# Optimization experiments

Hardware: AMD Instinct MI355X
Metric: run time of the kernel (lower is better)

## Reference

```python
import jax, jax.numpy as jnp
import numpy as np
from jax import lax

# Resolved Optuna hyperparameters
NPOINTS = (512, 256, 128)
RADII = (0.2, 0.4, 0.8)
KS = (32, 32, 32)
BN_EPS = 1e-5


def _fps_single(pts, npoint):
    """Farthest point sampling on one cloud. pts: (N,3) -> (npoint,) int32."""
    N = pts.shape[0]
    def step(carry, _):
        dists, last = carry
        d = jnp.sum((pts - pts[last]) ** 2, axis=-1)
        dists = jnp.minimum(dists, d)
        nxt = jnp.argmax(dists).astype(jnp.int32)
        return (dists, nxt), last
    init = (jnp.full((N,), 1e10, pts.dtype), jnp.int32(0))
    (_, _), idx = lax.scan(step, init, None, length=npoint)
    return idx


def _set_abstraction(xyz, feat, W, b, radius, k, npoint):
    """xyz: (B,N,3), feat: (B,N,C_in) -> new_xyz (B,S,3), new_feat (B,S,C_out)."""
    B, N, _ = xyz.shape
    fps_idx = jax.vmap(lambda p: _fps_single(p, npoint))(xyz)          # (B,S)
    new_xyz = jax.vmap(lambda x, i: x[i])(xyz, fps_idx)                # (B,S,3)
    # ball query: squared distances centers -> all points
    d2 = jnp.sum((new_xyz[:, :, None, :] - xyz[:, None, :, :]) ** 2, axis=-1)  # (B,S,N)
    valid = d2 <= radius * radius
    ar = jnp.arange(N, dtype=jnp.int32)
    gi = jnp.where(valid, ar[None, None, :], N)                        # invalid -> N
    gi = jnp.sort(gi, axis=-1)[:, :, :k]                               # first k in index order
    first = gi[:, :, :1]
    gi = jnp.where(gi == N, first, gi)                                 # pad with first valid (center itself)
    g_xyz = jax.vmap(lambda x, i: x[i])(xyz, gi)                       # (B,S,k,3)
    rel = g_xyz - new_xyz[:, :, None, :]
    g_feat = jax.vmap(lambda x, i: x[i])(feat, gi)                     # (B,S,k,C_in)
    h = jnp.concatenate([rel, g_feat], axis=-1)                        # (B,S,k,3+C_in)
    h = jax.nn.relu(jnp.einsum('bskc,co->bsko', h, W) + b)
    return new_xyz, jnp.max(h, axis=2)                                 # max-pool over group


def _bn(x, g, b):
    # nn.BatchNorm1d training-mode forward (batch statistics, biased var)
    m = x.mean(axis=0)
    v = x.var(axis=0)
    return (x - m) * lax.rsqrt(v + BN_EPS) * g + b


def setup_inputs() -> dict:
    key = jax.random.key(0)
    ks = jax.random.split(key, 8)
    def w(k, i, o):
        return (jax.random.normal(k, (i, o), jnp.float32) / np.sqrt(i)).astype(jnp.float32)
    return dict(
        points=jax.random.uniform(ks[0], (16, 4096, 3), jnp.float32),
        W1=w(ks[1], 3 + 3, 64),   b1=jnp.zeros((64,), jnp.float32),
        W2=w(ks[2], 64 + 3, 128), b2=jnp.zeros((128,), jnp.float32),
        W3=w(ks[3], 128 + 3, 256), b3=jnp.zeros((256,), jnp.float32),
        fc1_w=w(ks[4], 256, 256), fc1_b=jnp.zeros((256,), jnp.float32),
        fc2_w=w(ks[5], 256, 128), fc2_b=jnp.zeros((128,), jnp.float32),
        fc3_w=w(ks[6], 128, 12),  fc3_b=jnp.zeros((12,), jnp.float32),
        bn1_g=jnp.ones((256,), jnp.float32), bn1_b=jnp.zeros((256,), jnp.float32),
        bn2_g=jnp.ones((128,), jnp.float32), bn2_b=jnp.zeros((128,), jnp.float32),
    )


def reference(points, W1, b1, W2, b2, W3, b3, fc1_w, fc1_b, fc2_w, fc2_b,
              fc3_w, fc3_b, bn1_g, bn1_b, bn2_g, bn2_b):
    B = points.shape[0]
    xyz, feat = points, points
    for (W, bb, r, k, s) in ((W1, b1, RADII[0], KS[0], NPOINTS[0]),
                             (W2, b2, RADII[1], KS[1], NPOINTS[1]),
                             (W3, b3, RADII[2], KS[2], NPOINTS[2])):
        xyz, feat = _set_abstraction(xyz, feat, W, bb, r, k, s)
    f = jnp.max(feat, axis=1)                                          # (B, ch3)
    x = jax.nn.relu(_bn(f @ fc1_w + fc1_b, bn1_g, bn1_b))              # dropout: eval-mode identity
    x = jax.nn.relu(_bn(x @ fc2_w + fc2_b, bn2_g, bn2_b))
    x = x @ fc3_w + fc3_b
    return x.reshape(B, 4, 3)
```

## Files before the change

### kernel.cpp

```cpp
#include <hip/hip_runtime.h>
#include <hip/hip_bf16.h>


#define B_SZ 16

template<int CTRL>
__device__ __forceinline__ float dpp_mv(float v) {
    const int i = __float_as_int(v);
    const int r = __builtin_amdgcn_update_dpp(i, i, CTRL, 0xf, 0xf, false);
    return __int_as_float(r);
}

__device__ __forceinline__ float wave_max_f32(float x) {
    float v = x;
    v = fmaxf(v, dpp_mv<0x111>(v));
    v = fmaxf(v, dpp_mv<0x112>(v));
    v = fmaxf(v, dpp_mv<0x114>(v));
    v = fmaxf(v, dpp_mv<0x118>(v));
    v = fmaxf(v, dpp_mv<0x142>(v));
    v = fmaxf(v, dpp_mv<0x143>(v));
    return __uint_as_float(__builtin_amdgcn_readlane(__float_as_uint(v), 63));
}

__device__ __forceinline__ float read_lane_f32(float v, int l) {
    return __uint_as_float(__builtin_amdgcn_readlane(__float_as_uint(v), l));
}

template<int N, int NPOINT, int BLOCK, int S0, int S1, bool FIRST>
__global__ __launch_bounds__(BLOCK) void fps_kernel(
    const float* __restrict__ xyz,
    float* __restrict__ newxyz,
    float* __restrict__ dstate)
{
    constexpr int P  = N / BLOCK;
    constexpr int NW = BLOCK / 64;
    constexpr int O0 = FIRST ? 0 : S0;
    __shared__ float4 part[2][NW];
    __shared__ float  outb[(S1 - O0) * 3];

    const int b = blockIdx.x, tid = threadIdx.x;
    const int lane = tid & 63, w = tid >> 6;
    const float* xb = xyz + (size_t)b * N * 3;

    float px[P], py[P], pz[P], dd[P];
    const int base = tid * P;
#pragma unroll
    for (int i = 0; i < P; i++) {
        px[i] = xb[(base + i) * 3 + 0];
        py[i] = xb[(base + i) * 3 + 1];
        pz[i] = xb[(base + i) * 3 + 2];
    }
    float lx, ly, lz;
    if (FIRST) {
#pragma unroll
        for (int i = 0; i < P; i++) dd[i] = 1e10f;
        lx = xb[0]; ly = xb[1]; lz = xb[2];
        if (tid == 0) { outb[0] = lx; outb[1] = ly; outb[2] = lz; }
    } else {
#pragma unroll
        for (int i = 0; i < P; i++) dd[i] = dstate[((size_t)b * P + i) * BLOCK + tid];
        const float* c = newxyz + ((size_t)b * NPOINT + (S0 - 1)) * 3;
        lx = c[0]; ly = c[1]; lz = c[2];
    }

    for (int s = S0; s < S1; s++) {
        float bv = -1.0f, bx = 0.0f, by = 0.0f, bz = 0.0f;
#pragma unroll
        for (int i = 0; i < P; i++) {
            const float dx = px[i] - lx, dy = py[i] - ly, dz = pz[i] - lz;
            const float d2 = __fadd_rn(__fadd_rn(__fmul_rn(dx, dx), __fmul_rn(dy, dy)),
                                       __fmul_rn(dz, dz));
            const float nd = fminf(dd[i], d2);
            dd[i] = nd;
            const bool gt = nd > bv;
            bv = gt ? nd : bv;
            bx = gt ? px[i] : bx;
            by = gt ? py[i] : by;
            bz = gt ? pz[i] : bz;
        }
        const float wmax = wave_max_f32(bv);
        const unsigned long long mset = __ballot(bv == wmax);
        const int li = __ffsll(mset) - 1;
        const int buf = s & 1;
        if (lane == li) part[buf][w] = make_float4(bv, bx, by, bz);
        __syncthreads();
        float cv = -1.0f;
#pragma unroll
        for (int q = 0; q < NW; q++) {
            const float4 pq = part[buf][q];
            const bool gt = pq.x > cv;
            cv = gt ? pq.x : cv;
            lx = gt ? pq.y : lx;
            ly = gt ? pq.z : ly;
            lz = gt ? pq.w : lz;
        }
        if (tid == 0) {
            const int t = (s - O0) * 3;
            outb[t + 0] = lx; outb[t + 1] = ly; outb[t + 2] = lz;
        }
    }
    __syncthreads();
    if (S1 < NPOINT) {
#pragma unroll
        for (int i = 0; i < P; i++)
            dstate[((size_t)b * P + i) * BLOCK + tid] = dd[i];
    }
    float* o = newxyz + ((size_t)b * NPOINT + O0) * 3;
    for (int t = tid; t < (S1 - O0) * 3; t += BLOCK) o[t] = outb[t];
}

template<int N, int NPOINT>
__device__ __forceinline__ void fps_wave_body(
    const float* __restrict__ xyz,
    float* __restrict__ newxyz,
    const int b, const int lane)
{
    constexpr int P = N / 64;
    const float* xb = xyz + (size_t)b * N * 3;

    float px[P], py[P], pz[P], dd[P];
    const int base = lane * P;
#pragma unroll
    for (int i = 0; i < P; i++) {
        px[i] = xb[(base + i) * 3 + 0];
        py[i] = xb[(base + i) * 3 + 1];
        pz[i] = xb[(base + i) * 3 + 2];
        dd[i] = 1e10f;
    }
#pragma unroll
    for (int i = 0; i < P; i++) {
        asm volatile("" : "+v"(px[i]), "+v"(py[i]), "+v"(pz[i]));
    }
    float lx = xb[0], ly = xb[1], lz = xb[2];
    if (lane == 0) {
        float* o = newxyz + (size_t)b * NPOINT * 3;
        o[0] = lx; o[1] = ly; o[2] = lz;
    }

    for (int s = 1; s < NPOINT; s++) {
        float bv = -1.0f, bx = 0.0f, by = 0.0f, bz = 0.0f;
#pragma unroll
        for (int i = 0; i < P; i++) {
            const float dx = px[i] - lx, dy = py[i] - ly, dz = pz[i] - lz;
            const float d2 = __fadd_rn(__fadd_rn(__fmul_rn(dx, dx), __fmul_rn(dy, dy)),
                                       __fmul_rn(dz, dz));
            const float nd = fminf(dd[i], d2);
            dd[i] = nd;
            const bool gt = nd > bv;
            bv = gt ? nd : bv;
            bx = gt ? px[i] : bx;
            by = gt ? py[i] : by;
            bz = gt ? pz[i] : bz;
        }
        const float wmax = wave_max_f32(bv);
        const unsigned long long mset = __ballot(bv == wmax);
        const int li = __ffsll(mset) - 1;
        lx = read_lane_f32(bx, li);
        ly = read_lane_f32(by, li);
        lz = read_lane_f32(bz, li);
        if (lane == 0) {
            float* o = newxyz + ((size_t)b * NPOINT + s) * 3;
            o[0] = lx; o[1] = ly; o[2] = lz;
        }
    }
}

template<int N, int S, int CF, int COUT, int R, bool AMAX>
__device__ __forceinline__ void sa_body(
    const float* __restrict__ xyz,
    const float* __restrict__ feat,
    const float* __restrict__ cent,
    const float* __restrict__ W,
    const float* __restrict__ bias,
    float* __restrict__ outf,
    const float r2, const int s, const int b, const int lane)
{
    constexpr int K    = 32;
    constexpr int JT   = 16;
    constexpr int CIN  = CF + 3;
    constexpr int CINP = (CIN + 3) & ~3;
    constexpr int C4   = CIN & ~3;
    __shared__ int   gi[K];
    __shared__ float h[JT * CINP];

    const float* xb = xyz  + (size_t)b * N * 3;
    const float* fb = feat + (size_t)b * N * CF;
    const float cx = cent[((size_t)b * S + s) * 3 + 0];
    const float cy = cent[((size_t)b * S + s) * 3 + 1];
    const float cz = cent[((size_t)b * S + s) * 3 + 2];

    constexpr int RND = N / 256;
    int total = 0, g0 = 0;
    for (int r0 = 0; r0 < RND; r0++) {
        if (total >= K) break;
        float xs[4], ys[4], zs[4];
#pragma unroll
        for (int c4 = 0; c4 < 4; c4++) {
            const int p = (r0 * 4 + c4) * 64 + lane;
            xs[c4] = xb[p * 3 + 0];
            ys[c4] = xb[p * 3 + 1];
            zs[c4] = xb[p * 3 + 2];
        }
#pragma unroll
        for (int c4 = 0; c4 < 4; c4++) {
            const int p = (r0 * 4 + c4) * 64 + lane;
            const float dx = xs[c4] - cx, dy = ys[c4] - cy, dz = zs[c4] - cz;
            const float d2 = __fadd_rn(__fadd_rn(__fmul_rn(dx, dx), __fmul_rn(dy, dy)),
                                       __fmul_rn(dz, dz));
            const bool v = (d2 <= r2);
            const unsigned long long bal = __ballot(v);
            if (total == 0 && bal != 0ull) g0 = (r0 * 4 + c4) * 64 + (__ffsll(bal) - 1);
            const int pos = total + __popcll(bal & ((1ull << lane) - 1ull));
            if (v && pos < K) gi[pos] = p;
            total += __popcll(bal);
        }
    }
    if (lane == 0 && total < K) {
        for (int q = total; q < K; q++) gi[q] = g0;
    }
    __syncthreads();

    float m[R];
#pragma unroll
    for (int r = 0; r < R; r++) m[r] = -1e30f;

    for (int pass = 0; pass < K / JT; pass++) {
        for (int jj = 0; jj < JT; jj++) {
            const int idx = gi[pass * JT + jj];
            for (int c = lane; c < CIN; c += 64) {
                float val;
                if (c < 3) {
                    const float cc = (c == 0) ? cx : ((c == 1) ? cy : cz);
                    val = xb[idx * 3 + c] - cc;
                } else {
                    val = fb[(size_t)idx * CF + (c - 3)];
                }
                h[jj * CINP + c] = val;
            }
        }
        __syncthreads();

        float acc[JT][R];
#pragma unroll
        for (int jj = 0; jj < JT; jj++)
#pragma unroll
            for (int r = 0; r < R; r++) acc[jj][r] = 0.0f;

        const float* wp = W + lane;
        int c = 0;
        for (; c < C4; c += 4) {
            float wv[4][R];
#pragma unroll
            for (int q = 0; q < 4; q++)
#pragma unroll
                for (int r = 0; r < R; r++)
                    wv[q][r] = wp[(size_t)(c + q) * COUT + r * 64];
#pragma unroll
            for (int jj = 0; jj < JT; jj++) {
                const float4 hv = *(const float4*)&h[jj * CINP + c];
#pragma unroll
                for (int r = 0; r < R; r++) {
                    acc[jj][r] = fmaf(hv.x, wv[0][r], acc[jj][r]);
                    acc[jj][r] = fmaf(hv.y, wv[1][r], acc[jj][r]);
                    acc[jj][r] = fmaf(hv.z, wv[2][r], acc[jj][r]);
                    acc[jj][r] = fmaf(hv.w, wv[3][r], acc[jj][r]);
                }
            }
        }
        for (; c < CIN; c++) {
            float wv[R];
#pragma unroll
            for (int r = 0; r < R; r++) wv[r] = wp[(size_t)c * COUT + r * 64];
#pragma unroll
            for (int jj = 0; jj < JT; jj++) {
                const float hv = h[jj * CINP + c];
#pragma unroll
                for (int r = 0; r < R; r++)
                    acc[jj][r] = fmaf(hv, wv[r], acc[jj][r]);
            }
        }
#pragma unroll
        for (int jj = 0; jj < JT; jj++)
#pragma unroll
            for (int r = 0; r < R; r++) m[r] = fmaxf(m[r], acc[jj][r]);
        __syncthreads();
    }

#pragma unroll
    for (int r = 0; r < R; r++) {
        const int o = r * 64 + lane;
        const float val = fmaxf(bias[o] + m[r], 0.0f);
        if (AMAX) {
            atomicMax((unsigned*)&outf[(size_t)b * COUT + o], __float_as_uint(val));
        } else {
            outf[((size_t)b * S + s) * COUT + o] = val;
        }
    }
}

template<int N, int S, int CF, int COUT, int R, bool AMAX>
__global__ __launch_bounds__(64) void sa_kernel(
    const float* __restrict__ xyz, const float* __restrict__ feat,
    const float* __restrict__ cent, const float* __restrict__ W,
    const float* __restrict__ bias, float* __restrict__ outf, const float r2)
{
    sa_body<N, S, CF, COUT, R, AMAX>(xyz, feat, cent, W, bias, outf, r2,
                                     blockIdx.x, blockIdx.y, threadIdx.x);
}

template<int NF, int NPF, int N, int S, int CF, int COUT, int R>
__global__ __launch_bounds__(64) void fused_fps_sa_kernel(
    const float* __restrict__ fxyz,
    float* __restrict__ fnew,
    const float* __restrict__ xyz, const float* __restrict__ feat,
    const float* __restrict__ cent, const float* __restrict__ W,
    const float* __restrict__ bias, float* __restrict__ outf, const float r2)
{
    if (blockIdx.x < B_SZ) {
        __builtin_amdgcn_s_setprio(3);
        fps_wave_body<NF, NPF>(fxyz, fnew, blockIdx.x, threadIdx.x);
    } else {
        const int i = blockIdx.x - B_SZ;
        sa_body<N, S, CF, COUT, R, false>(xyz, feat, cent, W, bias, outf, r2,
                                          i % S, i / S, threadIdx.x);
    }
}

__global__ __launch_bounds__(64) void fc1_kernel(
    const float* __restrict__ f,
    const float* __restrict__ w,
    const float* __restrict__ bias,
    float* __restrict__ x1h)
{
    const int r = blockIdx.x >> 2;
    const int o = (blockIdx.x & 3) * 64 + threadIdx.x;
    const float* fr = f + r * 256;
    float acc = bias[o];
    for (int c = 0; c < 256; c += 4) {
        acc = fmaf(fr[c + 0], w[(size_t)(c + 0) * 256 + o], acc);
        acc = fmaf(fr[c + 1], w[(size_t)(c + 1) * 256 + o], acc);
        acc = fmaf(fr[c + 2], w[(size_t)(c + 2) * 256 + o], acc);
        acc = fmaf(fr[c + 3], w[(size_t)(c + 3) * 256 + o], acc);
    }
    x1h[r * 256 + o] = acc;
}

__global__ __launch_bounds__(256) void head2_kernel(
    const float* __restrict__ x1h,
    const float* __restrict__ fc2_w, const float* __restrict__ fc2_b,
    const float* __restrict__ fc3_w, const float* __restrict__ fc3_b,
    const float* __restrict__ bn1_g, const float* __restrict__ bn1_b,
    const float* __restrict__ bn2_g, const float* __restrict__ bn2_b,
    float* __restrict__ out)
{
    __shared__ float x1[16 * 257];
    __shared__ float x2[16 * 129];
    const int tid = threadIdx.x;

    for (int idx = tid; idx < 16 * 256; idx += 256) {
        const int r = idx >> 8, c = idx & 255;
        x1[r * 257 + c] = x1h[idx];
    }
    __syncthreads();
    {
        const int o = tid;
        float v[16];
#pragma unroll
        for (int r = 0; r < 16; r++) v[r] = x1[r * 257 + o];
        float m = 0.0f;
#pragma unroll
        for (int r = 0; r < 16; r++) m += v[r];
        m *= (1.0f / 16.0f);
        float var = 0.0f;
#pragma unroll
        for (int r = 0; r < 16; r++) { const float d = v[r] - m; var += d * d; }
        var *= (1.0f / 16.0f);
        const float sc = bn1_g[o] / sqrtf(var + 1e-5f);
        const float sh = bn1_b[o];
#pragma unroll
        for (int r = 0; r < 16; r++)
            x1[r * 257 + o] = fmaxf((v[r] - m) * sc + sh, 0.0f);
    }
    __syncthreads();
    {
        const int r = tid >> 4, g = tid & 15;
        float acc[8];
#pragma unroll
        for (int i = 0; i < 8; i++) acc[i] = fc2_b[g * 8 + i];
        const float* wrow = fc2_w + g * 8;
        for (int c = 0; c < 256; c++) {
            const float fv = x1[r * 257 + c];
            const float4* w4 = (const float4*)(wrow + (size_t)c * 128);
#pragma unroll
            for (int q = 0; q < 2; q++) {
                const float4 wv = w4[q];
                acc[q * 4 + 0] = fmaf(fv, wv.x, acc[q * 4 + 0]);
                acc[q * 4 + 1] = fmaf(fv, wv.y, acc[q * 4 + 1]);
                acc[q * 4 + 2] = fmaf(fv, wv.z, acc[q * 4 + 2]);
                acc[q * 4 + 3] = fmaf(fv, wv.w, acc[q * 4 + 3]);
            }
        }
#pragma unroll
        for (int i = 0; i < 8; i++) x2[r * 129 + g * 8 + i] = acc[i];
    }
    __syncthreads();
    if (tid < 128) {
        const int o = tid;
        float v[16];
#pragma unroll
        for (int r = 0; r < 16; r++) v[r] = x2[r * 129 + o];
        float m = 0.0f;
#pragma unroll
        for (int r = 0; r < 16; r++) m += v[r];
        m *= (1.0f / 16.0f);
        float var = 0.0f;
#pragma unroll
        for (int r = 0; r < 16; r++) { const float d = v[r] - m; var += d * d; }
        var *= (1.0f / 16.0f);
        const float sc = bn2_g[o] / sqrtf(var + 1e-5f);
        const float sh = bn2_b[o];
#pragma unroll
        for (int r = 0; r < 16; r++)
            x2[r * 129 + o] = fmaxf((v[r] - m) * sc + sh, 0.0f);
    }
    __syncthreads();
    if (tid < 192) {
        const int r = tid / 12, j = tid - r * 12;
        float acc = fc3_b[j];
        for (int c = 0; c < 128; c++)
            acc = fmaf(x2[r * 129 + c], fc3_w[c * 12 + j], acc);
        out[r * 12 + j] = acc;
    }
}

extern "C" void kernel_launch(void* const* d_in, const int* in_sizes, int n_in,
                              void* d_out, int out_size, void* d_ws, size_t ws_size,
                              hipStream_t stream) {
    const float* points = (const float*)d_in[0];
    const float* W1     = (const float*)d_in[1];
    const float* b1     = (const float*)d_in[2];
    const float* W2     = (const float*)d_in[3];
    const float* b2     = (const float*)d_in[4];
    const float* W3     = (const float*)d_in[5];
    const float* b3     = (const float*)d_in[6];
    const float* fc1_w  = (const float*)d_in[7];
    const float* fc1_b  = (const float*)d_in[8];
    const float* fc2_w  = (const float*)d_in[9];
    const float* fc2_b  = (const float*)d_in[10];
    const float* fc3_w  = (const float*)d_in[11];
    const float* fc3_b  = (const float*)d_in[12];
    const float* bn1_g  = (const float*)d_in[13];
    const float* bn1_b  = (const float*)d_in[14];
    const float* bn2_g  = (const float*)d_in[15];
    const float* bn2_b  = (const float*)d_in[16];
    float* out = (float*)d_out;

    float* ws   = (float*)d_ws;
    float* nx1  = ws;
    float* f1   = nx1 + 24576;
    float* nx2  = f1  + 524288;
    float* f2   = nx2 + 12288;
    float* nx3  = f2  + 524288;
    float* fmx  = nx3 + 6144;
    float* fdd  = fmx + 4096;
    float* x1h  = fdd + 65536;

    fps_kernel<4096, 512, 512, 1, 256, true><<<B_SZ, 512, 0, stream>>>(
        points, nx1, fdd);
    fps_kernel<4096, 512, 512, 256, 512, false><<<B_SZ, 512, 0, stream>>>(
        points, nx1, fdd);
    fused_fps_sa_kernel<512, 256, 4096, 512, 3, 64, 1>
        <<<B_SZ + 512 * B_SZ, 64, 0, stream>>>(
        nx1, nx2, points, points, nx1, W1, b1, f1, (float)(0.2 * 0.2));
    fused_fps_sa_kernel<256, 128, 512, 256, 64, 128, 2>
        <<<B_SZ + 256 * B_SZ, 64, 0, stream>>>(
        nx2, nx3, nx1, f1, nx2, W2, b2, f2, (float)(0.4 * 0.4));
    hipMemsetAsync(fmx, 0, 16 * 256 * sizeof(float), stream);
    sa_kernel<256, 128, 128, 256, 4, true><<<dim3(128, B_SZ), 64, 0, stream>>>(
        nx2, f2, nx3, W3, b3, fmx, (float)(0.8 * 0.8));
    fc1_kernel<<<64, 64, 0, stream>>>(fmx, fc1_w, fc1_b, x1h);
    head2_kernel<<<1, 256, 0, stream>>>(x1h, fc2_w, fc2_b, fc3_w, fc3_b,
                                        bn1_g, bn1_b, bn2_g, bn2_b, out);
}
```

Measured before the change: 717.2 us.

## Move FPS point coordinates to LDS and use packed float2 distance math

The farthest-point-sampling kernel now stages point coordinates in shared memory as packed float2 pairs instead of per-thread register arrays. Distance updates use two-wide vector math, meant to map onto packed FP32 instructions. The per-thread argmax becomes a tree max followed by an index search, and the cross-wave reduction exchanges only (value, index), with the winner's coordinates read back from LDS. This is meant to cut register pressure and the per-point select chains. In exchange it adds LDS reads every iteration, and the index decode hardcodes P=8 and H=4.

Measured after the change: 872.0 us. 1.22x slower.

```diff
diff --git a/kernel.cpp b/kernel.cpp
--- a/kernel.cpp
+++ b/kernel.cpp
@@ -3,6 +3,8 @@
 
 
 #define B_SZ 16
+
+typedef float vf2 __attribute__((ext_vector_type(2)));
 
 template<int CTRL>
 __device__ __forceinline__ float dpp_mv(float v) {
@@ -33,67 +35,106 @@
     float* __restrict__ dstate)
 {
     constexpr int P  = N / BLOCK;
+    constexpr int H  = P / 2;
     constexpr int NW = BLOCK / 64;
     constexpr int O0 = FIRST ? 0 : S0;
-    __shared__ float4 part[2][NW];
+    __shared__ vf2    xs2[H * BLOCK];
+    __shared__ vf2    ys2[H * BLOCK];
+    __shared__ vf2    zs2[H * BLOCK];
+    __shared__ float2 part[2][NW];
     __shared__ float  outb[(S1 - O0) * 3];
 
     const int b = blockIdx.x, tid = threadIdx.x;
     const int lane = tid & 63, w = tid >> 6;
     const float* xb = xyz + (size_t)b * N * 3;
 
-    float px[P], py[P], pz[P], dd[P];
-    const int base = tid * P;
-#pragma unroll
-    for (int i = 0; i < P; i++) {
-        px[i] = xb[(base + i) * 3 + 0];
-        py[i] = xb[(base + i) * 3 + 1];
-        pz[i] = xb[(base + i) * 3 + 2];
-    }
+    for (int idx = tid; idx < N / 2; idx += BLOCK) {
+        const int t = idx / H, g = idx - t * H;
+        const int p = idx * 2;
+        xs2[g * BLOCK + t] = (vf2){xb[p * 3 + 0], xb[(p + 1) * 3 + 0]};
+        ys2[g * BLOCK + t] = (vf2){xb[p * 3 + 1], xb[(p + 1) * 3 + 1]};
+        zs2[g * BLOCK + t] = (vf2){xb[p * 3 + 2], xb[(p + 1) * 3 + 2]};
+    }
+
+    vf2 dd2[H];
     float lx, ly, lz;
     if (FIRST) {
 #pragma unroll
-        for (int i = 0; i < P; i++) dd[i] = 1e10f;
+        for (int g = 0; g < H; g++) dd2[g] = (vf2){1e10f, 1e10f};
         lx = xb[0]; ly = xb[1]; lz = xb[2];
         if (tid == 0) { outb[0] = lx; outb[1] = ly; outb[2] = lz; }
     } else {
-#pragma unroll
-        for (int i = 0; i < P; i++) dd[i] = dstate[((size_t)b * P + i) * BLOCK + tid];
+        const vf2* ds = (const vf2*)dstate;
+#pragma unroll
+        for (int g = 0; g < H; g++)
+            dd2[g] = ds[((size_t)b * H + g) * BLOCK + tid];
         const float* c = newxyz + ((size_t)b * NPOINT + (S0 - 1)) * 3;
         lx = c[0]; ly = c[1]; lz = c[2];
     }
-
+    __syncthreads();
+
+    const int base = tid * P;
     for (int s = S0; s < S1; s++) {
-        float bv = -1.0f, bx = 0.0f, by = 0.0f, bz = 0.0f;
-#pragma unroll
-        for (int i = 0; i < P; i++) {
-            const float dx = px[i] - lx, dy = py[i] - ly, dz = pz[i] - lz;
-            const float d2 = __fadd_rn(__fadd_rn(__fmul_rn(dx, dx), __fmul_rn(dy, dy)),
-                                       __fmul_rn(dz, dz));
-            const float nd = fminf(dd[i], d2);
-            dd[i] = nd;
-            const bool gt = nd > bv;
-            bv = gt ? nd : bv;
-            bx = gt ? px[i] : bx;
-            by = gt ? py[i] : by;
-            bz = gt ? pz[i] : bz;
-        }
-        const float wmax = wave_max_f32(bv);
-        const unsigned long long mset = __ballot(bv == wmax);
+        {
+#pragma clang fp contract(off)
+            const vf2 lx2 = {lx, lx}, ly2 = {ly, ly}, lz2 = {lz, lz};
+#pragma unroll
+            for (int g = 0; g < H; g++) {
+                const vf2 xv = xs2[g * BLOCK + tid];
+                const vf2 yv = ys2[g * BLOCK + tid];
+                const vf2 zv = zs2[g * BLOCK + tid];
+                const vf2 dx = xv - lx2;
+                const vf2 dy = yv - ly2;
+                const vf2 dz = zv - lz2;
+                const vf2 t0 = dx * dx;
+                const vf2 t1 = dy * dy;
+                const vf2 t2 = dz * dz;
+                const vf2 d2 = (t0 + t1) + t2;
+                dd2[g].x = fminf(dd2[g].x, d2.x);
+                dd2[g].y = fminf(dd2[g].y, d2.y);
+            }
+        }
+        float pm[H];
+#pragma unroll
+        for (int g = 0; g < H; g++) pm[g] = fmaxf(dd2[g].x, dd2[g].y);
+#pragma unroll
+        for (int st = H / 2; st > 0; st >>= 1)
+#pragma unroll
+            for (int g = 0; g < H; g++)
+                if (g < st) pm[g] = fmaxf(pm[g], pm[g + st]);
+        const float tm = pm[0];
+
+        unsigned mm = 0u;
+#pragma unroll
+        for (int g = 0; g < H; g++) {
+            mm |= (dd2[g].x == tm) ? (1u << (2 * g)) : 0u;
+            mm |= (dd2[g].y == tm) ? (1u << (2 * g + 1)) : 0u;
+        }
+        const int g = base + (__ffs(mm) - 1);
+
+        const float wmax = wave_max_f32(tm);
+        const unsigned long long mset = __ballot(tm == wmax);
         const int li = __ffsll(mset) - 1;
         const int buf = s & 1;
-        if (lane == li) part[buf][w] = make_float4(bv, bx, by, bz);
+        if (lane == li) part[buf][w] = make_float2(wmax, __int_as_float(g));
         __syncthreads();
+
         float cv = -1.0f;
+        int gw = 0;
 #pragma unroll
         for (int q = 0; q < NW; q++) {
-            const float4 pq = part[buf][q];
+            const float2 pq = part[buf][q];
             const bool gt = pq.x > cv;
             cv = gt ? pq.x : cv;
-            lx = gt ? pq.y : lx;
-            ly = gt ? pq.z : ly;
-            lz = gt ? pq.w : lz;
-        }
+            gw = gt ? __float_as_int(pq.y) : gw;
+        }
+        const int tt = gw >> 3, gg = (gw & 7) >> 1, cc = gw & 1;
+        const vf2 xv = xs2[gg * BLOCK + tt];
+        const vf2 yv = ys2[gg * BLOCK + tt];
+        const vf2 zv = zs2[gg * BLOCK + tt];
+        lx = cc ? xv.y : xv.x;
+        ly = cc ? yv.y : yv.x;
+        lz = cc ? zv.y : zv.x;
         if (tid == 0) {
             const int t = (s - O0) * 3;
             outb[t + 0] = lx; outb[t + 1] = ly; outb[t + 2] = lz;
@@ -101,9 +142,10 @@
     }
     __syncthreads();
     if (S1 < NPOINT) {
-#pragma unroll
-        for (int i = 0; i < P; i++)
-            dstate[((size_t)b * P + i) * BLOCK + tid] = dd[i];
+        vf2* ds = (vf2*)dstate;
+#pragma unroll
+        for (int g = 0; g < H; g++)
+            ds[((size_t)b * H + g) * BLOCK + tid] = dd2[g];
     }
     float* o = newxyz + ((size_t)b * NPOINT + O0) * 3;
     for (int t = tid; t < (S1 - O0) * 3; t += BLOCK) o[t] = outb[t];
```

## Overlap second FPS half with SA1 on first-half centroids

Applied to the files above, without the earlier changes.

Stage-1 farthest point sampling was already split into two kernels. The second half now runs inside a fused kernel whose extra blocks do set-abstraction for the first 256 centroids, which are already final. SA1 for the remaining centroids moves into the next fused kernel, alongside FPS2. Shared memory buffers are hoisted into the kernels so a 512-thread block can run 8 SA waves, each with private scratch. This hides SA1 work behind the serial FPS chain, at the cost of 512-thread SA blocks competing with the FPS blocks for resources.

After: 709.1 us. Within noise of the previous version (-1.1%).

```diff
diff --git a/kernel.cpp b/kernel.cpp
--- a/kernel.cpp
+++ b/kernel.cpp
@@ -27,10 +27,11 @@
 }
 
 template<int N, int NPOINT, int BLOCK, int S0, int S1, bool FIRST>
-__global__ __launch_bounds__(BLOCK) void fps_kernel(
+__device__ __forceinline__ void fps_body(
     const float* __restrict__ xyz,
     float* __restrict__ newxyz,
-    float* __restrict__ dstate)
+    float* __restrict__ dstate,
+    const int b)
 {
     constexpr int P  = N / BLOCK;
     constexpr int NW = BLOCK / 64;
@@ -38,7 +39,7 @@
     __shared__ float4 part[2][NW];
     __shared__ float  outb[(S1 - O0) * 3];
 
-    const int b = blockIdx.x, tid = threadIdx.x;
+    const int tid = threadIdx.x;
     const int lane = tid & 63, w = tid >> 6;
     const float* xb = xyz + (size_t)b * N * 3;
 
@@ -109,6 +110,14 @@
     for (int t = tid; t < (S1 - O0) * 3; t += BLOCK) o[t] = outb[t];
 }
 
+template<int N, int NPOINT, int BLOCK, int S0, int S1, bool FIRST>
+__global__ __launch_bounds__(BLOCK) void fps_kernel(
+    const float* __restrict__ xyz, float* __restrict__ newxyz,
+    float* __restrict__ dstate)
+{
+    fps_body<N, NPOINT, BLOCK, S0, S1, FIRST>(xyz, newxyz, dstate, blockIdx.x);
+}
+
 template<int N, int NPOINT>
 __device__ __forceinline__ void fps_wave_body(
     const float* __restrict__ xyz,
@@ -173,15 +182,14 @@
     const float* __restrict__ W,
     const float* __restrict__ bias,
     float* __restrict__ outf,
-    const float r2, const int s, const int b, const int lane)
+    const float r2, const int s, const int b, const int lane,
+    int* __restrict__ gi, float* __restrict__ h)
 {
     constexpr int K    = 32;
     constexpr int JT   = 16;
     constexpr int CIN  = CF + 3;
     constexpr int CINP = (CIN + 3) & ~3;
     constexpr int C4   = CIN & ~3;
-    __shared__ int   gi[K];
-    __shared__ float h[JT * CINP];
 
     const float* xb = xyz  + (size_t)b * N * 3;
     const float* fb = feat + (size_t)b * N * CF;
@@ -304,11 +312,38 @@
     const float* __restrict__ cent, const float* __restrict__ W,
     const float* __restrict__ bias, float* __restrict__ outf, const float r2)
 {
+    constexpr int CINP = (CF + 3 + 3) & ~3;
+    __shared__ int   gi[32];
+    __shared__ float h[16 * CINP];
     sa_body<N, S, CF, COUT, R, AMAX>(xyz, feat, cent, W, bias, outf, r2,
-                                     blockIdx.x, blockIdx.y, threadIdx.x);
-}
-
-template<int NF, int NPF, int N, int S, int CF, int COUT, int R>
+                                     blockIdx.x, blockIdx.y, threadIdx.x, gi, h);
+}
+
+template<int N, int S, int CF, int COUT, int R, int SCNT>
+__global__ __launch_bounds__(512) void fused_fps1b_sa_kernel(
+    const float* __restrict__ fxyz, float* __restrict__ fnew,
+    float* __restrict__ fdd,
+    const float* __restrict__ xyz, const float* __restrict__ feat,
+    const float* __restrict__ cent, const float* __restrict__ W,
+    const float* __restrict__ bias, float* __restrict__ outf, const float r2)
+{
+    constexpr int CINP = (CF + 3 + 3) & ~3;
+    if (blockIdx.x < B_SZ) {
+        __builtin_amdgcn_s_setprio(3);
+        fps_body<4096, 512, 512, 256, 512, false>(fxyz, fnew, fdd, blockIdx.x);
+    } else {
+        __shared__ int   gi_s[8][32];
+        __shared__ float h_s[8][16 * CINP];
+        const int w = threadIdx.x >> 6, lane = threadIdx.x & 63;
+        const int widx = (blockIdx.x - B_SZ) * 8 + w;
+        const int b = widx / SCNT, s = widx % SCNT;
+        sa_body<N, S, CF, COUT, R, false>(xyz, feat, cent, W, bias, outf, r2,
+                                          s, b, lane, gi_s[w], h_s[w]);
+    }
+}
+
+template<int NF, int NPF, int N, int S, int CF, int COUT, int R,
+         int SOFF, int SCNT>
 __global__ __launch_bounds__(64) void fused_fps_sa_kernel(
     const float* __restrict__ fxyz,
     float* __restrict__ fnew,
@@ -316,13 +351,17 @@
     const float* __restrict__ cent, const float* __restrict__ W,
     const float* __restrict__ bias, float* __restrict__ outf, const float r2)
 {
+    constexpr int CINP = (CF + 3 + 3) & ~3;
     if (blockIdx.x < B_SZ) {
         __builtin_amdgcn_s_setprio(3);
         fps_wave_body<NF, NPF>(fxyz, fnew, blockIdx.x, threadIdx.x);
     } else {
+        __shared__ int   gi[32];
+        __shared__ float h[16 * CINP];
         const int i = blockIdx.x - B_SZ;
         sa_body<N, S, CF, COUT, R, false>(xyz, feat, cent, W, bias, outf, r2,
-                                          i % S, i / S, threadIdx.x);
+                                          SOFF + i % SCNT, i / SCNT,
+                                          threadIdx.x, gi, h);
     }
 }
 
@@ -467,12 +506,13 @@
 
     fps_kernel<4096, 512, 512, 1, 256, true><<<B_SZ, 512, 0, stream>>>(
         points, nx1, fdd);
-    fps_kernel<4096, 512, 512, 256, 512, false><<<B_SZ, 512, 0, stream>>>(
-        points, nx1, fdd);
-    fused_fps_sa_kernel<512, 256, 4096, 512, 3, 64, 1>
-        <<<B_SZ + 512 * B_SZ, 64, 0, stream>>>(
+    fused_fps1b_sa_kernel<4096, 512, 3, 64, 1, 256>
+        <<<B_SZ + 512, 512, 0, stream>>>(
+        points, nx1, fdd, points, points, nx1, W1, b1, f1, (float)(0.2 * 0.2));
+    fused_fps_sa_kernel<512, 256, 4096, 512, 3, 64, 1, 256, 256>
+        <<<B_SZ + 256 * B_SZ, 64, 0, stream>>>(
         nx1, nx2, points, points, nx1, W1, b1, f1, (float)(0.2 * 0.2));
-    fused_fps_sa_kernel<256, 128, 512, 256, 64, 128, 2>
+    fused_fps_sa_kernel<256, 128, 512, 256, 64, 128, 2, 0, 256>
         <<<B_SZ + 256 * B_SZ, 64, 0, stream>>>(
         nx2, nx3, nx1, f1, nx2, W2, b2, f2, (float)(0.4 * 0.4));
     hipMemsetAsync(fmx, 0, 16 * 256 * sizeof(float), stream);
```
